# Kernel optimization log

Hardware: AMD Instinct MI355X
Metric: run time of the kernel (lower is better)

The kernel has to match this reference:

```python
import jax, jax.numpy as jnp
import numpy as np

SHIFT, REDUCE = 3, 2
B, L, E, H = 64, 512, 300, 256


def _make_transitions():
    # Left-branching valid parse: S S R S R S R ... (L shifts, L-1 reduces)
    T = 2 * L - 1
    tr = np.full(T, REDUCE, dtype=np.int64)
    tr[0] = SHIFT
    tr[1::2] = SHIFT
    return jnp.asarray(np.tile(tr[None, :], (B, 1)))


def setup_inputs() -> dict:
    key = jax.random.key(0)
    ks = jax.random.split(key, 5)
    s = 0.05
    return {
        "sentence": jax.random.normal(ks[0], (B, L, E), jnp.float32),
        "transitions": _make_transitions(),
        "W_word": jax.random.normal(ks[1], (E, 2 * H), jnp.float32) * s,
        "b_word": jnp.zeros((2 * H,), jnp.float32),
        "W_left": jax.random.normal(ks[2], (H, 5 * H), jnp.float32) * s,
        "W_right": jax.random.normal(ks[3], (H, 5 * H), jnp.float32) * s,
        "b_reduce": jnp.zeros((5 * H,), jnp.float32),
    }


def reference(sentence, transitions, W_word, b_word, W_left, W_right, b_reduce):
    Bsz, Ls, _ = sentence.shape
    Hs = W_left.shape[0]
    proj = sentence @ W_word + b_word                  # [B, L, 2H] (word projection; BN/dropout disabled)
    h_buf, c_buf = jnp.split(proj, 2, axis=2)          # buffers, each [B, L, H]
    T = transitions.shape[1]
    bidx = jnp.arange(Bsz)

    def step(carry, trans_t):
        sh, sc, ptr, bp = carry                        # thin stacks [B,T+2,H], pointers [B]
        shift = trans_t == SHIFT
        i1 = jnp.maximum(ptr - 1, 0)                   # right child (stack top)
        i2 = jnp.maximum(ptr - 2, 0)                   # left child
        hl, cl = sh[bidx, i2], sc[bidx, i2]
        hr, cr = sh[bidx, i1], sc[bidx, i1]
        g = hl @ W_left + hr @ W_right + b_reduce      # [B, 5H] TreeLSTM gates
        ig, flg, frg, og, ug = jnp.split(g, 5, axis=1)
        c_red = (jax.nn.sigmoid(flg) * cl + jax.nn.sigmoid(frg) * cr
                 + jax.nn.sigmoid(ig) * jnp.tanh(ug))
        h_red = jax.nn.sigmoid(og) * jnp.tanh(c_red)
        bsafe = jnp.minimum(bp, Ls - 1)
        val_h = jnp.where(shift[:, None], h_buf[bidx, bsafe], h_red)
        val_c = jnp.where(shift[:, None], c_buf[bidx, bsafe], c_red)
        pos = jnp.where(shift, ptr, i2)                # shift pushes at ptr; reduce writes at ptr-2
        sh = sh.at[bidx, pos].set(val_h)
        sc = sc.at[bidx, pos].set(val_c)
        ptr = ptr + jnp.where(shift, 1, -1)
        bp = bp + shift.astype(bp.dtype)
        return (sh, sc, ptr, bp), None

    sh0 = jnp.zeros((Bsz, T + 2, Hs), sentence.dtype)
    sc0 = jnp.zeros((Bsz, T + 2, Hs), sentence.dtype)
    ptr0 = jnp.zeros((Bsz,), jnp.int32)
    bp0 = jnp.zeros((Bsz,), jnp.int32)
    (sh, sc, ptr, _), _ = jax.lax.scan(
        step, (sh0, sc0, ptr0, bp0), jnp.swapaxes(transitions, 0, 1))
    return sh[bidx, jnp.maximum(ptr - 1, 0)]           # final stack top h: [B, H]
```

## Files before the change

kernel.cpp:

```cpp
#include <hip/hip_runtime.h>
#include <hip/hip_bf16.h>
#include <math.h>

#define BSZ   64
#define LSEQ  512
#define EDIM  300
#define HDIM  256
#define TLEN  1023
#define PROJW 512
#define GW    1280

#define NROW  8
#define NHID  8
#define NRG   8
#define NBLK  256
#define SLOTS 2

#define PROJ_N   (BSZ*LSEQ*PROJW)
#define STACKF   PROJ_N
#define PAIRB    (STACKF/2)
#define PAIR_N   (2*BSZ*SLOTS*HDIM)
#define PAIR_CNT (2*BSZ*SLOTS*HDIM)

#define NODEBIT 0x80000000u
#define SENT    0xFFFFFFFFu
#define LROW    264
#define HRO     (NROW*LROW + 4)
#define RPITCH  328
#define RROW    41

__global__ void __launch_bounds__(256)
proj_gemm(const float* __restrict__ A, const float* __restrict__ W,
          const float* __restrict__ bias, float* __restrict__ out) {
    __shared__ float As[8][65];
    __shared__ float Bs[8][64];
    const int tid = threadIdx.x;
    const int tx = tid & 15, ty = tid >> 4;
    const int bm = blockIdx.y, bn = blockIdx.x;

    float acc[4][4] = {};
    const int e  = tid * 2;
    const int ar = e >> 3, ac = e & 7;
    const int br = e >> 6, bc = e & 63;

    for (int k0 = 0; k0 < EDIM; k0 += 8) {
        __syncthreads();
        {
            const float* Ap = A + (size_t)(bm * 64 + ar) * EDIM;
            int gk = k0 + ac;
            As[ac][ar]     = (gk     < EDIM) ? Ap[gk]     : 0.f;
            As[ac + 1][ar] = (gk + 1 < EDIM) ? Ap[gk + 1] : 0.f;
            int gkb = k0 + br;
            float w0 = 0.f, w1 = 0.f;
            if (gkb < EDIM) {
                const float* Wp = W + (size_t)gkb * PROJW + bn * 64;
                w0 = Wp[bc]; w1 = Wp[bc + 1];
            }
            Bs[br][bc] = w0; Bs[br][bc + 1] = w1;
        }
        __syncthreads();
        #pragma unroll
        for (int kk = 0; kk < 8; ++kk) {
            float a[4], b[4];
            #pragma unroll
            for (int i = 0; i < 4; ++i) a[i] = As[kk][ty * 4 + i];
            #pragma unroll
            for (int j = 0; j < 4; ++j) b[j] = Bs[kk][tx * 4 + j];
            #pragma unroll
            for (int i = 0; i < 4; ++i)
                #pragma unroll
                for (int j = 0; j < 4; ++j)
                    acc[i][j] += a[i] * b[j];
        }
    }
    #pragma unroll
    for (int i = 0; i < 4; ++i) {
        const int row  = bm * 64 + ty * 4 + i;
        const int col0 = bn * 64 + tx * 4;
        float* op = out + (size_t)row * PROJW + col0;
        #pragma unroll
        for (int j = 0; j < 4; ++j) op[j] = acc[i][j] + bias[col0 + j];
    }
}

__device__ __forceinline__ int qswz(int Q, int row) {
    return Q ^ row ^ ((Q >> 3) & 7);
}

__global__ void __launch_bounds__(256, 1)
scan_coop(const int* __restrict__ trans,
          const float* __restrict__ Wl, const float* __restrict__ Wr,
          const float* __restrict__ bred,
          float* __restrict__ ws, float* __restrict__ out) {
    __shared__ __align__(16) float hbuf[HRO + NROW * LROW];
    __shared__ __align__(16) float red[16 * RPITCH];
    __shared__ float    cstk[2 * SLOTS * NROW * NHID];
    __shared__ unsigned tbits[NROW][32];
    __shared__ unsigned fbits[32];
    __shared__ short    tg[NROW][SLOTS];
    __shared__ unsigned eps[NROW][SLOTS];
    __shared__ unsigned d_hl[NROW], d_hr[NROW], d_wr[NROW];
    __shared__ unsigned e_hl[NROW], e_hr[NROW];
    __shared__ unsigned c_l[NROW], c_r[NROW], cw[NROW];
    __shared__ unsigned d_oh[NROW], e_oh[NROW];
    __shared__ int      isred[NROW];

    const int tid   = threadIdx.x;
    const int rg    = blockIdx.x & 7;
    const int cs    = blockIdx.x >> 3;
    const int rbase = rg * NROW;
    const int n0    = cs * NHID;

    const int srow = tid >> 5, sc = tid & 31;
    const int colq = tid & 7;
    const int rh   = (tid >> 3) & 1;
    const int m    = (tid >> 4) & 1;
    const int w8   = tid >> 5;
    const int gn   = n0 + colq;
    const int orow = tid >> 3;

    unsigned long long* p64 = (unsigned long long*)ws;

    float4 w[8][5];
    {
        const float* src = (m == 0) ? Wl : Wr;
        const int kbase = w8 * 32;
        #pragma unroll
        for (int j = 0; j < 8; ++j) {
            const int k0 = kbase + j * 4;
            #pragma unroll
            for (int g = 0; g < 5; ++g) {
                w[j][g].x = src[(size_t)(k0 + 0) * GW + g * HDIM + gn];
                w[j][g].y = src[(size_t)(k0 + 1) * GW + g * HDIM + gn];
                w[j][g].z = src[(size_t)(k0 + 2) * GW + g * HDIM + gn];
                w[j][g].w = src[(size_t)(k0 + 3) * GW + g * HDIM + gn];
            }
        }
    }
    #pragma unroll
    for (int j = 0; j < 8; ++j)
        #pragma unroll
        for (int g = 0; g < 5; ++g)
            asm volatile("" : "+v"(w[j][g].x), "+v"(w[j][g].y),
                              "+v"(w[j][g].z), "+v"(w[j][g].w));

    if (tid < NROW * 32) {
        const int r2 = tid >> 5, wd = tid & 31;
        unsigned bits = 0;
        for (int j = 0; j < 32; ++j) {
            const int t = wd * 32 + j;
            if (t < TLEN && trans[(size_t)(rbase + r2) * TLEN + t] == 3) bits |= (1u << j);
        }
        tbits[r2][wd] = bits;
    }
    if (tid < NROW) {
        tg[tid][0] = -3; tg[tid][1] = -3;
        eps[tid][0] = 0; eps[tid][1] = 0;
        isred[tid] = 0;
    }
    __syncthreads();
    if (tid < 32) {
        unsigned fb = 0;
        #pragma unroll
        for (int r2 = 0; r2 < NROW; ++r2) fb |= ~tbits[r2][tid];
        if (tid == 31) fb &= 0x7FFFFFFFu;
        fbits[tid] = fb;
    }

    float bv[5];
    #pragma unroll
    for (int g = 0; g < 5; ++g) bv[g] = bred[g * HDIM + gn];

    int ptr = 0, bp = 0;
    unsigned nbar = 0;
    __syncthreads();

    for (int t = 0; t < TLEN; ++t) {
        const int redstep = (fbits[t >> 5] >> (t & 31)) & 1;
        if (redstep) ++nbar;

        if (tid < NROW) {
            const int r = tid, grow = rbase + r;
            const int is_shift = (tbits[r][t >> 5] >> (t & 31)) & 1;
            if (is_shift) {
                int pos = ptr; if (pos < 0) pos = 0; if (pos > SLOTS - 1) pos = SLOTS - 1;
                tg[r][pos] = (short)min(bp, LSEQ - 1);
                ptr++; bp++;
                isred[r] = 0;
            } else {
                const int i1 = min(max(ptr - 1, 0), SLOTS - 1);
                const int i2 = min(max(ptr - 2, 0), SLOTS - 1);
                const short t1 = tg[r][i1], t2 = tg[r][i2];
                unsigned dl, el = 0, cdl;
                if (t2 >= 0)       { dl = (unsigned)((grow * LSEQ + (int)t2) * PROJW); cdl = dl + HDIM; }
                else if (t2 <= -3) { dl = SENT; cdl = SENT; }
                else { const int par = (t2 == -2);
                       dl = NODEBIT | (unsigned)(PAIRB + ((par * BSZ + grow) * SLOTS + i2) * HDIM);
                       el = eps[r][i2];
                       cdl = NODEBIT | (unsigned)(par * 2 + i2); }
                unsigned dr, er = 0, cdr;
                if (t1 >= 0)       { dr = (unsigned)((grow * LSEQ + (int)t1) * PROJW); cdr = dr + HDIM; }
                else if (t1 <= -3) { dr = SENT; cdr = SENT; }
                else { const int par = (t1 == -2);
                       dr = NODEBIT | (unsigned)(PAIRB + ((par * BSZ + grow) * SLOTS + i1) * HDIM);
                       er = eps[r][i1];
                       cdr = NODEBIT | (unsigned)(par * 2 + i1); }
                d_hl[r] = dl; e_hl[r] = el; c_l[r] = cdl;
                d_hr[r] = dr; e_hr[r] = er; c_r[r] = cdr;
                const int pnew = (t2 == -1) ? 1 : 0;
                d_wr[r] = (unsigned)(PAIRB + ((pnew * BSZ + grow) * SLOTS + i2) * HDIM);
                cw[r]   = (unsigned)(pnew * 2 + i2);
                eps[r][i2] = nbar;
                tg[r][i2] = (short)(pnew ? -2 : -1);
                ptr--;
                isred[r] = 1;
            }
        }
        __syncthreads();

        if (!redstep) continue;

        if (isred[srow]) {
            #pragma unroll
            for (int buf = 0; buf < 2; ++buf) {
                float* hb = hbuf + buf * HRO;
                const unsigned oh = buf ? d_hr[srow] : d_hl[srow];
                const unsigned ee = buf ? e_hr[srow] : e_hl[srow];
                float h[8];
                if (oh == SENT) {
                    #pragma unroll
                    for (int i = 0; i < 8; ++i) h[i] = 0.f;
                } else if (!(oh & NODEBIT)) {
                    const float4 a = *(const float4*)(ws + oh + sc * 8);
                    const float4 b = *(const float4*)(ws + oh + sc * 8 + 4);
                    h[0]=a.x; h[1]=a.y; h[2]=a.z; h[3]=a.w;
                    h[4]=b.x; h[5]=b.y; h[6]=b.z; h[7]=b.w;
                } else {
                    const unsigned pb = (oh & ~NODEBIT) + sc * 8;
                    unsigned long long v[8];
                    for (;;) {
                        #pragma unroll
                        for (int i = 0; i < 8; ++i)
                            v[i] = __hip_atomic_load(p64 + pb + i,
                                     __ATOMIC_RELAXED, __HIP_MEMORY_SCOPE_AGENT);
                        bool ok = true;
                        #pragma unroll
                        for (int i = 0; i < 8; ++i)
                            ok &= ((unsigned)(v[i] >> 32) >= ee);
                        if (ok) break;
                        __builtin_amdgcn_s_sleep(1);
                    }
                    #pragma unroll
                    for (int i = 0; i < 8; ++i) h[i] = __uint_as_float((unsigned)v[i]);
                }
                *(float4*)&hb[srow * LROW + 4 * qswz(2 * sc + 0, srow)] =
                    make_float4(h[0], h[1], h[2], h[3]);
                *(float4*)&hb[srow * LROW + 4 * qswz(2 * sc + 1, srow)] =
                    make_float4(h[4], h[5], h[6], h[7]);
            }
        }
        __syncthreads();

        float clw = 0.f, crw = 0.f;
        if (tid < 64 && isred[orow]) {
            const unsigned cdl = c_l[orow], cdr = c_r[orow];
            if (cdl != SENT && !(cdl & NODEBIT)) clw = ws[cdl + gn];
            if (cdr != SENT && !(cdr & NODEBIT)) crw = ws[cdr + gn];
        }

        float acc[4][5];
        #pragma unroll
        for (int r = 0; r < 4; ++r)
            #pragma unroll
            for (int g = 0; g < 5; ++g) acc[r][g] = 0.f;
        {
            const float* hb = hbuf + m * HRO;
            #pragma unroll
            for (int j = 0; j < 8; ++j) {
                const int kq = w8 * 8 + j;
                #pragma unroll
                for (int r = 0; r < 4; ++r) {
                    const int row = rh * 4 + r;
                    const float4 x = *(const float4*)&hb[row * LROW + 4 * qswz(kq, row)];
                    #pragma unroll
                    for (int g = 0; g < 5; ++g)
                        acc[r][g] += x.x * w[j][g].x + x.y * w[j][g].y
                                   + x.z * w[j][g].z + x.w * w[j][g].w;
                }
            }
        }
        {
            const int g16 = w8 * 2 + m;
            #pragma unroll
            for (int r = 0; r < 4; ++r) {
                const int row = rh * 4 + r;
                #pragma unroll
                for (int g = 0; g < 5; ++g)
                    red[g16 * RPITCH + row * RROW + colq * 5 + g] = acc[r][g];
            }
        }
        __syncthreads();

        if (tid < 64) {
            if (isred[orow]) {
                float s[5];
                #pragma unroll
                for (int g = 0; g < 5; ++g) s[g] = bv[g];
                #pragma unroll
                for (int q = 0; q < 16; ++q)
                    #pragma unroll
                    for (int g = 0; g < 5; ++g)
                        s[g] += red[q * RPITCH + orow * RROW + colq * 5 + g];
                const unsigned cdl = c_l[orow], cdr = c_r[orow];
                const float cl = (cdl == SENT) ? 0.f :
                    ((cdl & NODEBIT) ? cstk[((cdl & 3) * NROW + orow) * NHID + colq] : clw);
                const float cr = (cdr == SENT) ? 0.f :
                    ((cdr & NODEBIT) ? cstk[((cdr & 3) * NROW + orow) * NHID + colq] : crw);
                const float si = 1.f / (1.f + expf(-s[0]));
                const float sl = 1.f / (1.f + expf(-s[1]));
                const float sr = 1.f / (1.f + expf(-s[2]));
                const float so = 1.f / (1.f + expf(-s[3]));
                const float c_red = sl * cl + sr * cr + si * tanhf(s[4]);
                const float h_red = so * tanhf(c_red);
                cstk[(cw[orow] * NROW + orow) * NHID + colq] = c_red;
                const unsigned long long pv =
                    ((unsigned long long)nbar << 32) | (unsigned long long)__float_as_uint(h_red);
                __hip_atomic_store(p64 + d_wr[orow] + gn, pv,
                                   __ATOMIC_RELAXED, __HIP_MEMORY_SCOPE_AGENT);
            }
        }
    }

    if (tid < NROW) {
        const int top = min(max(ptr - 1, 0), SLOTS - 1);
        const short tt = tg[tid][top];
        const int grow = rbase + tid;
        if (tt >= 0)       { d_oh[tid] = (unsigned)((grow * LSEQ + (int)tt) * PROJW); e_oh[tid] = 0; }
        else if (tt <= -3) { d_oh[tid] = SENT; e_oh[tid] = 0; }
        else { const int par = (tt == -2);
               d_oh[tid] = NODEBIT | (unsigned)(PAIRB + ((par * BSZ + grow) * SLOTS + top) * HDIM);
               e_oh[tid] = eps[tid][top]; }
    }
    __syncthreads();
    if (tid < 64) {
        const unsigned oh = d_oh[orow];
        float v;
        if (oh == SENT) v = 0.f;
        else if (!(oh & NODEBIT)) v = ws[oh + gn];
        else {
            const unsigned pb = (oh & ~NODEBIT) + gn;
            const unsigned ee = e_oh[orow];
            unsigned long long pv;
            for (;;) {
                pv = __hip_atomic_load(p64 + pb, __ATOMIC_RELAXED, __HIP_MEMORY_SCOPE_AGENT);
                if ((unsigned)(pv >> 32) >= ee) break;
                __builtin_amdgcn_s_sleep(1);
            }
            v = __uint_as_float((unsigned)pv);
        }
        out[(size_t)(rbase + orow) * HDIM + gn] = v;
    }
}

extern "C" void kernel_launch(void* const* d_in, const int* in_sizes, int n_in,
                              void* d_out, int out_size, void* d_ws, size_t ws_size,
                              hipStream_t stream) {
    const float* sentence    = (const float*)d_in[0];
    const int*   transitions = (const int*)  d_in[1];
    const float* W_word      = (const float*)d_in[2];
    const float* b_word      = (const float*)d_in[3];
    const float* W_left      = (const float*)d_in[4];
    const float* W_right     = (const float*)d_in[5];
    const float* b_reduce    = (const float*)d_in[6];
    float* out  = (float*)d_out;
    float* ws_f = (float*)d_ws;

    hipMemsetAsync((char*)d_ws + (size_t)STACKF * 4, 0,
                   (size_t)PAIR_CNT * 8, stream);

    dim3 g1(PROJW / 64, (BSZ * LSEQ) / 64);
    proj_gemm<<<g1, 256, 0, stream>>>(sentence, W_word, b_word, ws_f);

    scan_coop<<<NBLK, 256, 0, stream>>>(transitions, W_left, W_right, b_reduce,
                                        ws_f, out);
}
```

Baseline: 2.818 ms.

## Replace shared-memory gate reduction with in-wave shuffle reduction per column

Each wave now owns one output column and splits K across its lanes, with the two matrices on the two half-waves. Partial gate sums are reduced with xor shuffles in a transpose-reduce pattern, so the shared 'red' buffer and one block-wide barrier per reduce step are gone. The left/right child loads are also issued together so both spin-waits overlap, and the cell-state buffer loads move ahead of the barrier. In exchange, each thread now holds 8 rows × 5 gates of accumulators and does more shuffles, which raises register pressure.

```diff
diff --git a/kernel.cpp b/kernel.cpp
--- a/kernel.cpp
+++ b/kernel.cpp
@@ -19,15 +19,12 @@
 #define PROJ_N   (BSZ*LSEQ*PROJW)
 #define STACKF   PROJ_N
 #define PAIRB    (STACKF/2)
-#define PAIR_N   (2*BSZ*SLOTS*HDIM)
 #define PAIR_CNT (2*BSZ*SLOTS*HDIM)
 
 #define NODEBIT 0x80000000u
 #define SENT    0xFFFFFFFFu
 #define LROW    264
 #define HRO     (NROW*LROW + 4)
-#define RPITCH  328
-#define RROW    41
 
 __global__ void __launch_bounds__(256)
 proj_gemm(const float* __restrict__ A, const float* __restrict__ W,
@@ -93,7 +90,6 @@
           const float* __restrict__ bred,
           float* __restrict__ ws, float* __restrict__ out) {
     __shared__ __align__(16) float hbuf[HRO + NROW * LROW];
-    __shared__ __align__(16) float red[16 * RPITCH];
     __shared__ float    cstk[2 * SLOTS * NROW * NHID];
     __shared__ unsigned tbits[NROW][32];
     __shared__ unsigned fbits[32];
@@ -112,22 +108,20 @@
     const int n0    = cs * NHID;
 
     const int srow = tid >> 5, sc = tid & 31;
-    const int colq = tid & 7;
-    const int rh   = (tid >> 3) & 1;
+    const int colq = tid >> 5;
     const int m    = (tid >> 4) & 1;
-    const int w8   = tid >> 5;
+    const int w16  = tid & 15;
     const int gn   = n0 + colq;
-    const int orow = tid >> 3;
+    const int lane = tid & 63;
 
     unsigned long long* p64 = (unsigned long long*)ws;
 
-    float4 w[8][5];
+    float4 w[4][5];
     {
-        const float* src = (m == 0) ? Wl : Wr;
-        const int kbase = w8 * 32;
-        #pragma unroll
-        for (int j = 0; j < 8; ++j) {
-            const int k0 = kbase + j * 4;
+        const float* src = m ? Wr : Wl;
+        #pragma unroll
+        for (int j = 0; j < 4; ++j) {
+            const int k0 = (w16 * 4 + j) * 4;
             #pragma unroll
             for (int g = 0; g < 5; ++g) {
                 w[j][g].x = src[(size_t)(k0 + 0) * GW + g * HDIM + gn];
@@ -138,7 +132,7 @@
         }
     }
     #pragma unroll
-    for (int j = 0; j < 8; ++j)
+    for (int j = 0; j < 4; ++j)
         #pragma unroll
         for (int g = 0; g < 5; ++g)
             asm volatile("" : "+v"(w[j][g].x), "+v"(w[j][g].y),
@@ -220,68 +214,101 @@
 
         if (!redstep) continue;
 
+        float clw = 0.f, crw = 0.f;
+        int frow = 0;
+        const bool fin = ((lane & 31) < 8);
+        if (fin) {
+            frow = ((lane & 1) << 2) | (lane & 2) | ((lane & 4) >> 2);
+            if (isred[frow]) {
+                const unsigned cdl = c_l[frow], cdr = c_r[frow];
+                if (cdl != SENT && !(cdl & NODEBIT)) clw = ws[cdl + gn];
+                if (cdr != SENT && !(cdr & NODEBIT)) crw = ws[cdr + gn];
+            }
+        }
+
         if (isred[srow]) {
-            #pragma unroll
-            for (int buf = 0; buf < 2; ++buf) {
-                float* hb = hbuf + buf * HRO;
-                const unsigned oh = buf ? d_hr[srow] : d_hl[srow];
-                const unsigned ee = buf ? e_hr[srow] : e_hl[srow];
-                float h[8];
-                if (oh == SENT) {
+            const unsigned oh0 = d_hl[srow], oh1 = d_hr[srow];
+            const unsigned ee0 = e_hl[srow], ee1 = e_hr[srow];
+            const bool nd0 = (oh0 != SENT) && (oh0 & NODEBIT);
+            const bool nd1 = (oh1 != SENT) && (oh1 & NODEBIT);
+            float h0[8], h1[8];
+
+            if (oh0 == SENT) {
+                #pragma unroll
+                for (int i = 0; i < 8; ++i) h0[i] = 0.f;
+            } else if (!nd0) {
+                const float4 a = *(const float4*)(ws + oh0 + sc * 8);
+                const float4 b = *(const float4*)(ws + oh0 + sc * 8 + 4);
+                h0[0]=a.x; h0[1]=a.y; h0[2]=a.z; h0[3]=a.w;
+                h0[4]=b.x; h0[5]=b.y; h0[6]=b.z; h0[7]=b.w;
+            }
+            if (oh1 == SENT) {
+                #pragma unroll
+                for (int i = 0; i < 8; ++i) h1[i] = 0.f;
+            } else if (!nd1) {
+                const float4 a = *(const float4*)(ws + oh1 + sc * 8);
+                const float4 b = *(const float4*)(ws + oh1 + sc * 8 + 4);
+                h1[0]=a.x; h1[1]=a.y; h1[2]=a.z; h1[3]=a.w;
+                h1[4]=b.x; h1[5]=b.y; h1[6]=b.z; h1[7]=b.w;
+            }
+            if (nd0) {
+                const unsigned pb = (oh0 & ~NODEBIT) + sc * 8;
+                unsigned long long v[8];
+                for (;;) {
                     #pragma unroll
-                    for (int i = 0; i < 8; ++i) h[i] = 0.f;
-                } else if (!(oh & NODEBIT)) {
-                    const float4 a = *(const float4*)(ws + oh + sc * 8);
-                    const float4 b = *(const float4*)(ws + oh + sc * 8 + 4);
-                    h[0]=a.x; h[1]=a.y; h[2]=a.z; h[3]=a.w;
-                    h[4]=b.x; h[5]=b.y; h[6]=b.z; h[7]=b.w;
-                } else {
-                    const unsigned pb = (oh & ~NODEBIT) + sc * 8;
-                    unsigned long long v[8];
-                    for (;;) {
-                        #pragma unroll
-                        for (int i = 0; i < 8; ++i)
-                            v[i] = __hip_atomic_load(p64 + pb + i,
-                                     __ATOMIC_RELAXED, __HIP_MEMORY_SCOPE_AGENT);
-                        bool ok = true;
-                        #pragma unroll
-                        for (int i = 0; i < 8; ++i)
-                            ok &= ((unsigned)(v[i] >> 32) >= ee);
-                        if (ok) break;
-                        __builtin_amdgcn_s_sleep(1);
-                    }
+                    for (int i = 0; i < 8; ++i)
+                        v[i] = __hip_atomic_load(p64 + pb + i,
+                                 __ATOMIC_RELAXED, __HIP_MEMORY_SCOPE_AGENT);
+                    bool ok = true;
                     #pragma unroll
-                    for (int i = 0; i < 8; ++i) h[i] = __uint_as_float((unsigned)v[i]);
+                    for (int i = 0; i < 8; ++i) ok &= ((unsigned)(v[i] >> 32) >= ee0);
+                    if (ok) break;
+                    __builtin_amdgcn_s_sleep(1);
                 }
-                *(float4*)&hb[srow * LROW + 4 * qswz(2 * sc + 0, srow)] =
-                    make_float4(h[0], h[1], h[2], h[3]);
-                *(float4*)&hb[srow * LROW + 4 * qswz(2 * sc + 1, srow)] =
-                    make_float4(h[4], h[5], h[6], h[7]);
-            }
+                #pragma unroll
+                for (int i = 0; i < 8; ++i) h0[i] = __uint_as_float((unsigned)v[i]);
+            }
+            if (nd1) {
+                const unsigned pb = (oh1 & ~NODEBIT) + sc * 8;
+                unsigned long long v[8];
+                for (;;) {
+                    #pragma unroll
+                    for (int i = 0; i < 8; ++i)
+                        v[i] = __hip_atomic_load(p64 + pb + i,
+                                 __ATOMIC_RELAXED, __HIP_MEMORY_SCOPE_AGENT);
+                    bool ok = true;
+                    #pragma unroll
+                    for (int i = 0; i < 8; ++i) ok &= ((unsigned)(v[i] >> 32) >= ee1);
+                    if (ok) break;
+                    __builtin_amdgcn_s_sleep(1);
+                }
+                #pragma unroll
+                for (int i = 0; i < 8; ++i) h1[i] = __uint_as_float((unsigned)v[i]);
+            }
+            *(float4*)&hbuf[srow * LROW + 4 * qswz(2 * sc + 0, srow)] =
+                make_float4(h0[0], h0[1], h0[2], h0[3]);
+            *(float4*)&hbuf[srow * LROW + 4 * qswz(2 * sc + 1, srow)] =
+                make_float4(h0[4], h0[5], h0[6], h0[7]);
+            *(float4*)&hbuf[HRO + srow * LROW + 4 * qswz(2 * sc + 0, srow)] =
+                make_float4(h1[0], h1[1], h1[2], h1[3]);
+            *(float4*)&hbuf[HRO + srow * LROW + 4 * qswz(2 * sc + 1, srow)] =
+                make_float4(h1[4], h1[5], h1[6], h1[7]);
         }
         __syncthreads();
 
-        float clw = 0.f, crw = 0.f;
-        if (tid < 64 && isred[orow]) {
-            const unsigned cdl = c_l[orow], cdr = c_r[orow];
-            if (cdl != SENT && !(cdl & NODEBIT)) clw = ws[cdl + gn];
-            if (cdr != SENT && !(cdr & NODEBIT)) crw = ws[cdr + gn];
-        }
-
-        float acc[4][5];
-        #pragma unroll
-        for (int r = 0; r < 4; ++r)
+        float acc[8][5];
+        #pragma unroll
+        for (int r = 0; r < 8; ++r)
             #pragma unroll
             for (int g = 0; g < 5; ++g) acc[r][g] = 0.f;
         {
             const float* hb = hbuf + m * HRO;
             #pragma unroll
-            for (int j = 0; j < 8; ++j) {
-                const int kq = w8 * 8 + j;
-                #pragma unroll
-                for (int r = 0; r < 4; ++r) {
-                    const int row = rh * 4 + r;
-                    const float4 x = *(const float4*)&hb[row * LROW + 4 * qswz(kq, row)];
+            for (int j = 0; j < 4; ++j) {
+                const int kq = w16 * 4 + j;
+                #pragma unroll
+                for (int r = 0; r < 8; ++r) {
+                    const float4 x = *(const float4*)&hb[r * LROW + 4 * qswz(kq, r)];
                     #pragma unroll
                     for (int g = 0; g < 5; ++g)
                         acc[r][g] += x.x * w[j][g].x + x.y * w[j][g].y
@@ -289,45 +316,72 @@
                 }
             }
         }
+
+        #pragma unroll
+        for (int r = 0; r < 8; ++r)
+            #pragma unroll
+            for (int g = 0; g < 5; ++g)
+                acc[r][g] += __shfl_xor(acc[r][g], 16);
+
+        float a4[4][5];
         {
-            const int g16 = w8 * 2 + m;
-            #pragma unroll
-            for (int r = 0; r < 4; ++r) {
-                const int row = rh * 4 + r;
-                #pragma unroll
-                for (int g = 0; g < 5; ++g)
-                    red[g16 * RPITCH + row * RROW + colq * 5 + g] = acc[r][g];
-            }
-        }
-        __syncthreads();
-
-        if (tid < 64) {
-            if (isred[orow]) {
-                float s[5];
-                #pragma unroll
-                for (int g = 0; g < 5; ++g) s[g] = bv[g];
-                #pragma unroll
-                for (int q = 0; q < 16; ++q)
-                    #pragma unroll
-                    for (int g = 0; g < 5; ++g)
-                        s[g] += red[q * RPITCH + orow * RROW + colq * 5 + g];
-                const unsigned cdl = c_l[orow], cdr = c_r[orow];
-                const float cl = (cdl == SENT) ? 0.f :
-                    ((cdl & NODEBIT) ? cstk[((cdl & 3) * NROW + orow) * NHID + colq] : clw);
-                const float cr = (cdr == SENT) ? 0.f :
-                    ((cdr & NODEBIT) ? cstk[((cdr & 3) * NROW + orow) * NHID + colq] : crw);
-                const float si = 1.f / (1.f + expf(-s[0]));
-                const float sl = 1.f / (1.f + expf(-s[1]));
-                const float sr = 1.f / (1.f + expf(-s[2]));
-                const float so = 1.f / (1.f + expf(-s[3]));
-                const float c_red = sl * cl + sr * cr + si * tanhf(s[4]);
-                const float h_red = so * tanhf(c_red);
-                cstk[(cw[orow] * NROW + orow) * NHID + colq] = c_red;
-                const unsigned long long pv =
-                    ((unsigned long long)nbar << 32) | (unsigned long long)__float_as_uint(h_red);
-                __hip_atomic_store(p64 + d_wr[orow] + gn, pv,
-                                   __ATOMIC_RELAXED, __HIP_MEMORY_SCOPE_AGENT);
-            }
+            const bool kl = ((lane & 1) == 0);
+            #pragma unroll
+            for (int r = 0; r < 4; ++r)
+                #pragma unroll
+                for (int g = 0; g < 5; ++g) {
+                    const float lo = acc[r][g], hi = acc[r + 4][g];
+                    const float sd = kl ? hi : lo;
+                    const float rc = __shfl_xor(sd, 1);
+                    a4[r][g] = (kl ? lo : hi) + rc;
+                }
+        }
+        float a2[2][5];
+        {
+            const bool kl = ((lane & 2) == 0);
+            #pragma unroll
+            for (int r = 0; r < 2; ++r)
+                #pragma unroll
+                for (int g = 0; g < 5; ++g) {
+                    const float lo = a4[r][g], hi = a4[r + 2][g];
+                    const float sd = kl ? hi : lo;
+                    const float rc = __shfl_xor(sd, 2);
+                    a2[r][g] = (kl ? lo : hi) + rc;
+                }
+        }
+        float a1[5];
+        {
+            const bool kl = ((lane & 4) == 0);
+            #pragma unroll
+            for (int g = 0; g < 5; ++g) {
+                const float lo = a2[0][g], hi = a2[1][g];
+                const float sd = kl ? hi : lo;
+                const float rc = __shfl_xor(sd, 4);
+                a1[g] = (kl ? lo : hi) + rc;
+            }
+        }
+        #pragma unroll
+        for (int g = 0; g < 5; ++g) a1[g] += __shfl_xor(a1[g], 8);
+
+        if (fin && isred[frow]) {
+            const unsigned cdl = c_l[frow], cdr = c_r[frow];
+            const float cl = (cdl == SENT) ? 0.f :
+                ((cdl & NODEBIT) ? cstk[((cdl & 3) * NROW + frow) * NHID + colq] : clw);
+            const float cr = (cdr == SENT) ? 0.f :
+                ((cdr & NODEBIT) ? cstk[((cdr & 3) * NROW + frow) * NHID + colq] : crw);
+            const float s0 = a1[0] + bv[0], s1 = a1[1] + bv[1], s2 = a1[2] + bv[2],
+                        s3 = a1[3] + bv[3], s4 = a1[4] + bv[4];
+            const float si = 1.f / (1.f + expf(-s0));
+            const float sl = 1.f / (1.f + expf(-s1));
+            const float sr = 1.f / (1.f + expf(-s2));
+            const float so = 1.f / (1.f + expf(-s3));
+            const float c_red = sl * cl + sr * cr + si * tanhf(s4);
+            const float h_red = so * tanhf(c_red);
+            cstk[(cw[frow] * NROW + frow) * NHID + colq] = c_red;
+            const unsigned long long pv =
+                ((unsigned long long)nbar << 32) | (unsigned long long)__float_as_uint(h_red);
+            __hip_atomic_store(p64 + d_wr[frow] + gn, pv,
+                               __ATOMIC_RELAXED, __HIP_MEMORY_SCOPE_AGENT);
         }
     }
 
@@ -343,12 +397,14 @@
     }
     __syncthreads();
     if (tid < 64) {
+        const int orow = tid >> 3;
+        const int ocol = n0 + (tid & 7);
         const unsigned oh = d_oh[orow];
         float v;
         if (oh == SENT) v = 0.f;
-        else if (!(oh & NODEBIT)) v = ws[oh + gn];
+        else if (!(oh & NODEBIT)) v = ws[oh + ocol];
         else {
-            const unsigned pb = (oh & ~NODEBIT) + gn;
+            const unsigned pb = (oh & ~NODEBIT) + ocol;
             const unsigned ee = e_oh[orow];
             unsigned long long pv;
             for (;;) {
@@ -358,7 +414,7 @@
             }
             v = __uint_as_float((unsigned)pv);
         }
-        out[(size_t)(rbase + orow) * HDIM + gn] = v;
+        out[(size_t)(rbase + orow) * HDIM + ocol] = v;
     }
 }
 
```

New measurement: 3.427 ms. 21.6% more time.
